# Optimization experiments

Hardware: AMD Instinct MI355X
Metric: run time of the kernel (lower is better)

Reference implementation:

```python
import jax, jax.numpy as jnp
import numpy as np

T, B = 50, 512
S, A, BEL, H, E, M = 256, 32, 1024, 1024, 1024, 256
MIN_STD = 0.1


def setup_inputs() -> dict:
    key = jax.random.key(0)
    ks = jax.random.split(key, 24)
    def rn(k, shape, scale=1.0):
        return jax.random.normal(k, shape, dtype=jnp.float32) * scale
    w = 0.05  # weight init scale
    return {
        "prev_state": rn(ks[0], (B, S)),
        "actions": rn(ks[1], (T, B, A)),
        "prev_belief": rn(ks[2], (B, BEL)),
        "observations": rn(ks[3], (T, B, E)),
        "nonterminals": jnp.ones((T, B, 1), dtype=jnp.float32),
        "map_embeddings": rn(ks[4], (T, B, M)),
        "map_embeddings_post": rn(ks[5], (T, B, M)),
        "noise_prior": rn(ks[6], (T, B, S)),
        "noise_post": rn(ks[7], (T, B, S)),
        "W_sa": rn(ks[8], (BEL, S + A + M), w), "b_sa": jnp.zeros((BEL,), jnp.float32),
        "W_ih": rn(ks[9], (3 * BEL, BEL), w), "b_ih": jnp.zeros((3 * BEL,), jnp.float32),
        "W_hh": rn(ks[10], (3 * BEL, BEL), w), "b_hh": jnp.zeros((3 * BEL,), jnp.float32),
        "W_bp": rn(ks[11], (H, BEL), w), "b_bp": jnp.zeros((H,), jnp.float32),
        "W_sp": rn(ks[12], (2 * S, H), w), "b_sp": jnp.zeros((2 * S,), jnp.float32),
        "W_bq": rn(ks[13], (H, BEL + E + M), w), "b_bq": jnp.zeros((H,), jnp.float32),
        "W_sq": rn(ks[14], (2 * S, H), w), "b_sq": jnp.zeros((2 * S,), jnp.float32),
    }


def reference(prev_state, actions, prev_belief, observations, nonterminals,
              map_embeddings, map_embeddings_post, noise_prior, noise_post,
              W_sa, b_sa, W_ih, b_ih, W_hh, b_hh,
              W_bp, b_bp, W_sp, b_sp, W_bq, b_bq, W_sq, b_sq):
    relu = jax.nn.relu
    def lin(x, W, b):
        return x @ W.T + b

    def gru(x, h):  # torch.nn.GRUCell math
        gi = x @ W_ih.T + b_ih
        gh = h @ W_hh.T + b_hh
        i_r, i_z, i_n = jnp.split(gi, 3, axis=1)
        h_r, h_z, h_n = jnp.split(gh, 3, axis=1)
        r = jax.nn.sigmoid(i_r + h_r)
        z = jax.nn.sigmoid(i_z + h_z)
        n = jnp.tanh(i_n + r * h_n)
        return (1.0 - z) * n + z * h

    def std(raw):
        return jnp.minimum(jax.nn.softplus(raw) + MIN_STD, 5.0)

    def step(carry, xs):
        belief, post_state = carry
        a, obs, nt, me, mp, np_, nq = xs
        s = post_state * nt
        hid = relu(lin(jnp.concatenate([s, a, me], axis=1), W_sa, b_sa))
        belief = gru(hid, belief)
        # prior p(z_t | h_t)
        hp = relu(lin(belief, W_bp, b_bp))
        p_mean, p_raw = jnp.split(lin(hp, W_sp, b_sp), 2, axis=1)
        p_std = std(p_raw)
        p_state = p_mean + p_std * np_
        # posterior q(z_t | h_t, e_t, m_t)
        hq = relu(lin(jnp.concatenate([belief, obs, mp], axis=1), W_bq, b_bq))
        q_mean, q_raw = jnp.split(lin(hq, W_sq, b_sq), 2, axis=1)
        q_std = std(q_raw)
        q_state = q_mean + q_std * nq
        return (belief, q_state), (belief, p_state, p_mean, p_std, q_state, q_mean, q_std)

    _, outs = jax.lax.scan(
        step, (prev_belief, prev_state),
        (actions, observations, nonterminals, map_embeddings,
         map_embeddings_post, noise_prior, noise_post))
    return outs  # 7 arrays, each (T, B, *)
```

## Files before the change

kernel.cpp:

```cpp
#include <hip/hip_runtime.h>
#include <hip/hip_bf16.h>

#define NT 50
#define NB 512
#define SD 256
#define BD 1024
#define HD 1024
#define ED 1024
#define MD 256
#define NBLK 512
#define PGSZ (1024 * 256)
#define K1BIG 0x40000000
#define WPRE_OFF 49152

typedef __attribute__((ext_vector_type(8))) short bf16x8;
typedef __attribute__((ext_vector_type(4))) float f32x4;

__device__ __forceinline__ void gload_lds16(const void* g, void* l) {
  __builtin_amdgcn_global_load_lds(
      (const __attribute__((address_space(1))) void*)g,
      (__attribute__((address_space(3))) void*)l, 16, 0, 0);
}
__device__ __forceinline__ void gload_lds16_sc0(const void* g, void* l) {
  __builtin_amdgcn_global_load_lds(
      (const __attribute__((address_space(1))) void*)g,
      (__attribute__((address_space(3))) void*)l, 16, 0, 1);
}

__device__ __forceinline__ void aload16(const void* a, f32x4* r) {
  asm volatile("global_load_dwordx4 %0, %1, off sc0" : "=&v"(*r) : "v"(a) : "memory");
}
__device__ __forceinline__ void aload4(const void* a, float* r) {
  asm volatile("global_load_dword %0, %1, off sc0" : "=&v"(*r) : "v"(a) : "memory");
}
#define VMWAIT(N)                                        \
  asm volatile("s_waitcnt vmcnt(" #N ")" ::: "memory");  \
  __builtin_amdgcn_sched_barrier(0);

__device__ __forceinline__ void astore16(void* g, f32x4 v) {
  asm volatile("global_store_dwordx4 %0, %1, off sc0" :: "v"(g), "v"(v) : "memory");
}
__device__ __forceinline__ void astore4(void* g, float v) {
  asm volatile("global_store_dword %0, %1, off sc0" :: "v"(g), "v"(v) : "memory");
}
__device__ __forceinline__ void astore2(void* g, unsigned v) {
  asm volatile("global_store_short %0, %1, off sc0" :: "v"(g), "v"(v) : "memory");
}
__device__ __forceinline__ void ntstore16(void* g, f32x4 v) {
  asm volatile("global_store_dwordx4 %0, %1, off nt" :: "v"(g), "v"(v) : "memory");
}
__device__ __forceinline__ void ntstore4(void* g, float v) {
  asm volatile("global_store_dword %0, %1, off nt" :: "v"(g), "v"(v) : "memory");
}

__device__ __forceinline__ float sigmoidf_(float x) { return 1.0f / (1.0f + __expf(-x)); }
__device__ __forceinline__ float softplusf_(float x) {
  return (x > 0.0f) ? (x + log1pf(__expf(-x))) : log1pf(__expf(x));
}
__device__ __forceinline__ unsigned short bfb(float x) {
  __hip_bfloat16 h = __float2bfloat16(x);
  return __builtin_bit_cast(unsigned short, h);
}

__device__ __forceinline__ void wpre_issue(const __hip_bfloat16* W, int ldw,
                                           char* lds, int tid) {
  const int w = tid >> 6, lane = tid & 63;
  const __hip_bfloat16* wrow = W + (size_t)lane * ldw;
  char* wpre = lds + WPRE_OFF;
#pragma unroll
  for (int c = 0; c < 3; ++c) {
    gload_lds16(wrow + (c << 6) + (2 * w) * 8, wpre + c * 8192 + (2 * w) * 1024);
    gload_lds16(wrow + (c << 6) + (2 * w + 1) * 8, wpre + c * 8192 + (2 * w + 1) * 1024);
  }
}

__device__ __forceinline__ void xbar_pf(unsigned* cnt, int inst, int xcd, int nx,
                                        const __hip_bfloat16* nextW, int nextLdw,
                                        char* lds, int tid) {
  asm volatile("s_waitcnt vmcnt(0) lgkmcnt(0)" ::: "memory");
  __syncthreads();
  unsigned* c = cnt + 256 + (size_t)(inst * 8 + xcd) * 16;
  if (tid == 0)
    __hip_atomic_fetch_add(c, 1u, __ATOMIC_RELAXED, __HIP_MEMORY_SCOPE_AGENT);
  if (nextW) wpre_issue(nextW, nextLdw, lds, tid);
  if (tid == 0) {
    while (__hip_atomic_load(c, __ATOMIC_RELAXED, __HIP_MEMORY_SCOPE_AGENT) < (unsigned)nx)
      __builtin_amdgcn_s_sleep(2);
  }
  __syncthreads();
}

__device__ __noinline__ void gemm64(
    int EPI, char* lds, bool pre,
    const __hip_bfloat16* __restrict__ A1, int lda1,
    const __hip_bfloat16* __restrict__ A2, int lda2, int K1,
    const __hip_bfloat16* __restrict__ Wr, int ldw, int nIter,
    const float* __restrict__ bias, const float* __restrict__ Cadd,
    float* __restrict__ Cf, __hip_bfloat16* __restrict__ Cb, int ldc, int m0) {
  const int tid = threadIdx.x;
  const int lane = tid & 63, w = tid >> 6;
  const int wr = w >> 1, wc = w & 1;
  f32x4 acc[2][2] = {};
  const __hip_bfloat16* a1r = A1 + (size_t)(m0 + lane) * lda1;
  const __hip_bfloat16* a2r = A2 ? (A2 + (size_t)(m0 + lane) * lda2) : a1r;
  const __hip_bfloat16* wrow = Wr + (size_t)lane * ldw;
  char* wpre = lds + WPRE_OFF;

  auto aissue = [&](int it) {
    const int k0 = it << 6;
    char* la = lds + (size_t)(it % 3) * 16384;
    const __hip_bfloat16* as = (k0 < K1) ? (a1r + k0) : (a2r + (k0 - K1));
    gload_lds16_sc0(as + (2 * w) * 8, la + (2 * w) * 1024);
    gload_lds16_sc0(as + (2 * w + 1) * 8, la + (2 * w + 1) * 1024);
  };
  auto stageAW = [&](int it) {
    const int k0 = it << 6;
    char* la = lds + (size_t)(it % 3) * 16384;
    char* lb = la + 8192;
    const __hip_bfloat16* as = (k0 < K1) ? (a1r + k0) : (a2r + (k0 - K1));
    gload_lds16_sc0(as + (2 * w) * 8, la + (2 * w) * 1024);
    gload_lds16_sc0(as + (2 * w + 1) * 8, la + (2 * w + 1) * 1024);
    gload_lds16(wrow + k0 + (2 * w) * 8, lb + (2 * w) * 1024);
    gload_lds16(wrow + k0 + (2 * w + 1) * 8, lb + (2 * w + 1) * 1024);
  };

  __syncthreads();
  if (!pre) wpre_issue(Wr, ldw, lds, tid);
  aissue(0);
  aissue(1);
  aissue(2);
  VMWAIT(4)
  __builtin_amdgcn_s_barrier();
  __builtin_amdgcn_sched_barrier(0);

  const int kq = lane >> 4, r15 = lane & 15;
  for (int i = 0; i < nIter; ++i) {
    const char* la = lds + (size_t)(i % 3) * 16384;
    const char* lb = (i < 3) ? (wpre + (size_t)i * 8192) : (la + 8192);
#pragma unroll
    for (int s = 0; s < 2; ++s) {
      bf16x8 af[2], bfr[2];
#pragma unroll
      for (int m = 0; m < 2; ++m)
        af[m] = *(const bf16x8*)(la + (size_t)((s * 4 + kq) * 64 + wr * 32 + m * 16 + r15) * 16);
#pragma unroll
      for (int n = 0; n < 2; ++n)
        bfr[n] = *(const bf16x8*)(lb + (size_t)((s * 4 + kq) * 64 + wc * 32 + n * 16 + r15) * 16);
#pragma unroll
      for (int m = 0; m < 2; ++m)
#pragma unroll
        for (int n = 0; n < 2; ++n)
          acc[m][n] = __builtin_amdgcn_mfma_f32_16x16x32_bf16(af[m], bfr[n], acc[m][n], 0, 0, 0);
    }
    if (i + 1 < nIter) {
      if (i == 0) {
        VMWAIT(2)
      } else if (i + 2 < nIter) {
        VMWAIT(4)
      } else {
        VMWAIT(0)
      }
      __builtin_amdgcn_s_barrier();
      __builtin_amdgcn_sched_barrier(0);
      if (i + 3 < nIter) stageAW(i + 3);
    }
  }

  const int rg = lane >> 4;
  float ad[2][2][4];
  if (EPI == 3) {
#pragma unroll
    for (int m = 0; m < 2; ++m)
#pragma unroll
      for (int n = 0; n < 2; ++n) {
        const int col = wc * 32 + n * 16 + r15;
#pragma unroll
        for (int i2 = 0; i2 < 4; ++i2) {
          const int row = m0 + wr * 32 + m * 16 + rg * 4 + i2;
          aload4(Cadd + (size_t)row * ldc + col, &ad[m][n][i2]);
        }
      }
    VMWAIT(0)
  }
#pragma unroll
  for (int m = 0; m < 2; ++m) {
#pragma unroll
    for (int n = 0; n < 2; ++n) {
      const int col = wc * 32 + n * 16 + r15;
      const float bv = bias ? bias[col] : 0.0f;
#pragma unroll
      for (int i2 = 0; i2 < 4; ++i2) {
        const int row = m0 + wr * 32 + m * 16 + rg * 4 + i2;
        float v = acc[m][n][i2] + bv;
        if (EPI == 3) v += ad[m][n][i2];
        if (EPI == 0) {
          astore4(Cf + (size_t)row * ldc + col, v);
        } else {
          v = v > 0.0f ? v : 0.0f;
          astore2(Cb + (size_t)row * ldc + col, (unsigned)bfb(v));
        }
      }
    }
  }
}

__device__ __noinline__ void gemm_head64(
    char* lds, bool pre, const __hip_bfloat16* __restrict__ A,
    const __hip_bfloat16* __restrict__ Wr, const float* __restrict__ bias,
    const float* __restrict__ noise, float* __restrict__ st_o, float* __restrict__ mn_o,
    float* __restrict__ sd_o, const float* __restrict__ ntn,
    __hip_bfloat16* __restrict__ sprev, int isq, int n0, int m0) {
  const int tid = threadIdx.x;
  const int lane = tid & 63, w = tid >> 6;
  const int wr = w >> 1, wc = w & 1;
  f32x4 acc[2][2] = {};
  const __hip_bfloat16* ar = A + (size_t)(m0 + lane) * BD;
  const __hip_bfloat16* wrow = Wr + (size_t)lane * BD;
  char* wpre = lds + WPRE_OFF;

  auto aissue = [&](int it) {
    const int k0 = it << 6;
    char* la = lds + (size_t)(it % 3) * 16384;
    gload_lds16_sc0(ar + k0 + (2 * w) * 8, la + (2 * w) * 1024);
    gload_lds16_sc0(ar + k0 + (2 * w + 1) * 8, la + (2 * w + 1) * 1024);
  };
  auto stageAW = [&](int it) {
    const int k0 = it << 6;
    char* la = lds + (size_t)(it % 3) * 16384;
    char* lb = la + 8192;
    gload_lds16_sc0(ar + k0 + (2 * w) * 8, la + (2 * w) * 1024);
    gload_lds16_sc0(ar + k0 + (2 * w + 1) * 8, la + (2 * w + 1) * 1024);
    gload_lds16(wrow + k0 + (2 * w) * 8, lb + (2 * w) * 1024);
    gload_lds16(wrow + k0 + (2 * w + 1) * 8, lb + (2 * w + 1) * 1024);
  };

  __syncthreads();
  if (!pre) wpre_issue(Wr, BD, lds, tid);
  aissue(0);
  aissue(1);
  aissue(2);
  VMWAIT(4)
  __builtin_amdgcn_s_barrier();
  __builtin_amdgcn_sched_barrier(0);

  const int kq = lane >> 4, r15 = lane & 15;
  for (int i = 0; i < 16; ++i) {
    const char* la = lds + (size_t)(i % 3) * 16384;
    const char* lb = (i < 3) ? (wpre + (size_t)i * 8192) : (la + 8192);
#pragma unroll
    for (int s = 0; s < 2; ++s) {
      bf16x8 af[2], bfr[2];
#pragma unroll
      for (int m = 0; m < 2; ++m)
        af[m] = *(const bf16x8*)(la + (size_t)((s * 4 + kq) * 64 + wr * 32 + m * 16 + r15) * 16);
#pragma unroll
      for (int n = 0; n < 2; ++n)
        bfr[n] = *(const bf16x8*)(lb + (size_t)((s * 4 + kq) * 64 + wc * 32 + n * 16 + r15) * 16);
#pragma unroll
      for (int m = 0; m < 2; ++m)
#pragma unroll
        for (int n = 0; n < 2; ++n)
          acc[m][n] = __builtin_amdgcn_mfma_f32_16x16x32_bf16(af[m], bfr[n], acc[m][n], 0, 0, 0);
    }
    if (i + 1 < 16) {
      if (i == 0) {
        VMWAIT(2)
      } else if (i + 2 < 16) {
        VMWAIT(4)
      } else {
        VMWAIT(0)
      }
      __builtin_amdgcn_s_barrier();
      __builtin_amdgcn_sched_barrier(0);
      if (i + 3 < 16) stageAW(i + 3);
    }
  }

  const int rg = lane >> 4;
  const bool even = (r15 & 1) == 0;
#pragma unroll
  for (int m = 0; m < 2; ++m) {
#pragma unroll
    for (int n = 0; n < 2; ++n) {
      const int col = n0 + wc * 32 + n * 16 + r15;
      const int j = col >> 1;
      const float bv = bias[col];
#pragma unroll
      for (int i2 = 0; i2 < 4; ++i2) {
        const int row = m0 + wr * 32 + m * 16 + rg * 4 + i2;
        float v = acc[m][n][i2] + bv;
        float partner = __shfl_xor(v, 1);
        float mean = even ? v : partner;
        float raw = even ? partner : v;
        float sd = fminf(softplusf_(raw) + 0.1f, 5.0f);
        const size_t o = (size_t)row * SD + j;
        if (even) {
          float st = mean + sd * noise[o];
          ntstore4(mn_o + o, mean);
          ntstore4(st_o + o, st);
          if (isq) astore2(sprev + o, (unsigned)bfb(st * ntn[row]));
        } else {
          ntstore4(sd_o + o, sd);
        }
      }
    }
  }
}

struct Args {
  const float *prev_state, *actions, *prev_belief, *observations, *nonterminals,
      *me, *mp, *noise_p, *noise_q,
      *W_sa, *b_sa, *W_ih, *b_ih, *W_hh, *b_hh,
      *W_bp, *b_bp, *W_sp, *b_sp, *W_bq, *b_bq, *W_sq, *b_sq;
  float* out;
  unsigned* cnt;
  __hip_bfloat16 *Wsa, *Wih, *Whh, *Wbp, *Wbq, *Wsp, *Wsq;
  __hip_bfloat16 *actme, *obsmp, *sprev, *bel, *hid, *hpb, *hqb;
  float *gi, *gh, *hq_obs;
  float *bsp_ro, *bsq_ro;
};

__global__ __launch_bounds__(256) void prep(Args P) {
  const int gtid = blockIdx.x * 256 + threadIdx.x;
  for (int i = gtid; i < BD * 576; i += PGSZ) {
    int r = i / 576, k = i - r * 576;
    P.Wsa[i] = __float2bfloat16(k < 544 ? P.W_sa[(size_t)r * 544 + k] : 0.0f);
  }
  for (int i = gtid; i < 3 * BD * BD; i += PGSZ) P.Wih[i] = __float2bfloat16(P.W_ih[i]);
  for (int i = gtid; i < 3 * BD * BD; i += PGSZ) P.Whh[i] = __float2bfloat16(P.W_hh[i]);
  for (int i = gtid; i < HD * BD; i += PGSZ) P.Wbp[i] = __float2bfloat16(P.W_bp[i]);
  for (int i = gtid; i < HD * 2304; i += PGSZ) P.Wbq[i] = __float2bfloat16(P.W_bq[i]);
  for (int i = gtid; i < 512 * HD; i += PGSZ) {
    int r = i >> 10, k = i & 1023;
    int dr = (r < 256) ? (2 * r) : (2 * (r - 256) + 1);
    P.Wsp[(size_t)dr * 1024 + k] = __float2bfloat16(P.W_sp[i]);
    P.Wsq[(size_t)dr * 1024 + k] = __float2bfloat16(P.W_sq[i]);
  }
  for (int i = gtid; i < 512; i += PGSZ) {
    int dr = (i < 256) ? (2 * i) : (2 * (i - 256) + 1);
    P.bsp_ro[dr] = P.b_sp[i];
    P.bsq_ro[dr] = P.b_sq[i];
  }
  for (int i = gtid; i < NT * NB * 320; i += PGSZ) {
    int tb = i / 320, j = i - tb * 320;
    float v = (j < 32) ? P.actions[(size_t)tb * 32 + j]
                       : (j < 288 ? P.me[(size_t)tb * 256 + (j - 32)] : 0.0f);
    P.actme[i] = __float2bfloat16(v);
  }
  for (int i = gtid; i < NB * 1280; i += PGSZ) {
    int bb = i / 1280, j = i - bb * 1280;
    float v = (j < ED) ? P.observations[(size_t)bb * ED + j] : P.mp[(size_t)bb * MD + (j - ED)];
    P.obsmp[i] = __float2bfloat16(v);
  }
  for (int i = gtid; i < NB * SD; i += PGSZ) {
    int r = i >> 8;
    P.sprev[i] = __float2bfloat16(P.prev_state[i] * P.nonterminals[r]);
  }
  for (int i = gtid; i < NB * BD; i += PGSZ) P.bel[i] = __float2bfloat16(P.prev_belief[i]);
}

__global__ __launch_bounds__(256, 2) void mega(Args P) {
  __shared__ alignas(16) char lds[73728];
  __shared__ int sh[4];
  const int tid = threadIdx.x;

  if (tid == 0) {
    unsigned x;
    asm volatile("s_getreg_b32 %0, hwreg(HW_REG_XCC_ID)" : "=s"(x));
    x &= 7u;
    unsigned s = __hip_atomic_fetch_add(P.cnt + x * 16, 1u, __ATOMIC_RELAXED,
                                        __HIP_MEMORY_SCOPE_AGENT);
    sh[0] = (int)x;
    sh[1] = (int)s;
  }
  __syncthreads();
  const int xcd = sh[0], slot = sh[1];

  if (tid == 0) {
    __hip_atomic_fetch_add(P.cnt + 128, 1u, __ATOMIC_RELAXED, __HIP_MEMORY_SCOPE_AGENT);
    while (__hip_atomic_load(P.cnt + 128, __ATOMIC_RELAXED, __HIP_MEMORY_SCOPE_AGENT) <
           (unsigned)NBLK)
      __builtin_amdgcn_s_sleep(4);
    sh[2] = (int)__hip_atomic_load(P.cnt + xcd * 16, __ATOMIC_RELAXED,
                                   __HIP_MEMORY_SCOPE_AGENT);
  }
  __syncthreads();
  const int nx = sh[2];
  const int m0 = xcd * 64;
  const size_t o_ps = (size_t)NT * NB * BD;
  const size_t blk = (size_t)NT * NB * SD;

  const __hip_bfloat16* wA = nullptr; int lA = 0;
  if (slot < 16) { wA = P.Wsa + (size_t)slot * 64 * 576; lA = 576; }
  else if (slot < 64) { wA = P.Whh + (size_t)(slot - 16) * 64 * BD; lA = BD; }
  const __hip_bfloat16* wB = nullptr; int lB = 0;
  if (slot < 48) { wB = P.Wih + (size_t)slot * 64 * BD; lB = BD; }
  else if (slot < 64) { wB = P.Wbq + (size_t)(slot - 48) * 64 * 2304 + 1024; lB = 2304; }
  const __hip_bfloat16* wD = nullptr; int lD = 0;
  if (slot < 16) { wD = P.Wbp + (size_t)slot * 64 * BD; lD = BD; }
  else if (slot < 32) { wD = P.Wbq + (size_t)(slot - 16) * 64 * 2304; lD = 2304; }
  const __hip_bfloat16* wE = nullptr; int lE = 0;
  if (slot < 8) { wE = P.Wsp + (size_t)slot * 64 * BD; lE = BD; }
  else if (slot < 16) { wE = P.Wsq + (size_t)(slot - 8) * 64 * BD; lE = BD; }

  if (wA) wpre_issue(wA, lA, lds, tid);

  for (int t = 0; t < NT; ++t) {
    const int inst = t * 5;
    for (int tt = slot; tt < 64; tt += nx) {
      const bool pre = (tt == slot);
      if (tt < 16) {
        gemm64(1, lds, pre, P.sprev, SD, P.actme + (size_t)t * NB * 320, 320, 256,
               P.Wsa + (size_t)tt * 64 * 576, 576, 9,
               P.b_sa + tt * 64, nullptr, nullptr, P.hid + tt * 64, BD, m0);
      } else {
        const int n = tt - 16;
        gemm64(0, lds, pre, P.bel, BD, nullptr, 0, K1BIG,
               P.Whh + (size_t)n * 64 * BD, BD, 16,
               P.b_hh + n * 64, nullptr, P.gh + n * 64, nullptr, 3 * BD, m0);
      }
    }
    xbar_pf(P.cnt, inst + 0, xcd, nx, wB, lB, lds, tid);
    for (int tt = slot; tt < 64; tt += nx) {
      const bool pre = (tt == slot);
      if (tt < 48) {
        gemm64(0, lds, pre, P.hid, BD, nullptr, 0, K1BIG,
               P.Wih + (size_t)tt * 64 * BD, BD, 16,
               P.b_ih + tt * 64, nullptr, P.gi + tt * 64, nullptr, 3 * BD, m0);
      } else {
        const int n = tt - 48;
        gemm64(0, lds, pre, P.obsmp, 1280, nullptr, 0, K1BIG,
               P.Wbq + (size_t)n * 64 * 2304 + 1024, 2304, 20,
               nullptr, nullptr, P.hq_obs + n * 64, nullptr, 1024, m0);
      }
    }
    xbar_pf(P.cnt, inst + 1, xcd, nx, wD, lD, lds, tid);
    for (int u = slot * 256 + tid; u < 8192; u += nx * 256) {
      const int r = m0 + (u >> 7), j0 = (u & 127) << 3;
      const float* gib = P.gi + (size_t)r * 3072 + j0;
      const float* ghb = P.gh + (size_t)r * 3072 + j0;
      f32x4 ir0, ir1, iz0, iz1, in0, in1, hr0, hr1, hz0, hz1, hn0, hn1, hbv;
      aload16(gib, &ir0);
      aload16(gib + 4, &ir1);
      aload16(gib + 1024, &iz0);
      aload16(gib + 1028, &iz1);
      aload16(gib + 2048, &in0);
      aload16(gib + 2052, &in1);
      aload16(ghb, &hr0);
      aload16(ghb + 4, &hr1);
      aload16(ghb + 1024, &hz0);
      aload16(ghb + 1028, &hz1);
      aload16(ghb + 2048, &hn0);
      aload16(ghb + 2052, &hn1);
      aload16(P.bel + (size_t)r * BD + j0, &hbv);
      VMWAIT(0)
      bf16x8 hb = __builtin_bit_cast(bf16x8, hbv);
      float o[8];
      unsigned short nb[8];
#pragma unroll
      for (int k = 0; k < 8; ++k) {
        float gr = (k < 4 ? ir0[k] : ir1[k - 4]) + (k < 4 ? hr0[k] : hr1[k - 4]);
        float gz = (k < 4 ? iz0[k] : iz1[k - 4]) + (k < 4 ? hz0[k] : hz1[k - 4]);
        float hn = (k < 4 ? hn0[k] : hn1[k - 4]);
        float in_ = (k < 4 ? in0[k] : in1[k - 4]);
        float r_ = sigmoidf_(gr);
        float z_ = sigmoidf_(gz);
        float n_ = tanhf(in_ + r_ * hn);
        __hip_bfloat16 hv16 = __builtin_bit_cast(__hip_bfloat16, (unsigned short)hb[k]);
        float hv = __bfloat162float(hv16);
        float bel = (1.0f - z_) * n_ + z_ * hv;
        o[k] = bel;
        nb[k] = bfb(bel);
      }
      float* ob = P.out + (size_t)t * NB * BD + (size_t)r * BD + j0;
      ntstore16(ob, f32x4{o[0], o[1], o[2], o[3]});
      ntstore16(ob + 4, f32x4{o[4], o[5], o[6], o[7]});
      astore16(P.bel + (size_t)r * BD + j0, __builtin_bit_cast(f32x4, *(bf16x8*)nb));
    }
    if (t + 1 < NT) {
      for (int v = slot * 256 + tid; v < 5120; v += nx * 256) {
        const int r = m0 + v / 80, c0 = (v % 80) << 4;
        const float* src = (c0 < ED)
            ? (P.observations + (size_t)(t + 1) * NB * ED + (size_t)r * ED + c0)
            : (P.mp + (size_t)(t + 1) * NB * MD + (size_t)r * MD + (c0 - ED));
        unsigned short nb[16];
#pragma unroll
        for (int q = 0; q < 4; ++q) {
          f32x4 vv = *(const f32x4*)(src + q * 4);
#pragma unroll
          for (int kk = 0; kk < 4; ++kk) nb[q * 4 + kk] = bfb(vv[kk]);
        }
        astore16(P.obsmp + (size_t)r * 1280 + c0, __builtin_bit_cast(f32x4, *(bf16x8*)nb));
        astore16(P.obsmp + (size_t)r * 1280 + c0 + 8,
                 __builtin_bit_cast(f32x4, *(bf16x8*)(nb + 8)));
      }
    }
    xbar_pf(P.cnt, inst + 2, xcd, nx, nullptr, 0, lds, tid);
    for (int tt = slot; tt < 32; tt += nx) {
      const bool pre = (tt == slot);
      if (tt < 16) {
        gemm64(1, lds, pre, P.bel, BD, nullptr, 0, K1BIG,
               P.Wbp + (size_t)tt * 64 * BD, BD, 16,
               P.b_bp + tt * 64, nullptr, nullptr, P.hpb + tt * 64, HD, m0);
      } else {
        const int n = tt - 16;
        gemm64(3, lds, pre, P.bel, BD, nullptr, 0, K1BIG,
               P.Wbq + (size_t)n * 64 * 2304, 2304, 16,
               P.b_bq + n * 64, P.hq_obs + n * 64, nullptr, P.hqb + n * 64, HD, m0);
      }
    }
    xbar_pf(P.cnt, inst + 3, xcd, nx, wE, lE, lds, tid);
    {
      const float* ntn = P.nonterminals + (size_t)((t + 1 < NT) ? t + 1 : t) * NB;
      const size_t to = (size_t)t * NB * SD;
      for (int tt = slot; tt < 16; tt += nx) {
        const bool pre = (tt == slot);
        if (tt < 8)
          gemm_head64(lds, pre, P.hpb, P.Wsp + (size_t)tt * 64 * BD, P.bsp_ro,
                      P.noise_p + to, P.out + o_ps + to, P.out + o_ps + blk + to,
                      P.out + o_ps + 2 * blk + to, ntn, P.sprev, 0, tt * 64, m0);
        else
          gemm_head64(lds, pre, P.hqb, P.Wsq + (size_t)(tt - 8) * 64 * BD, P.bsq_ro,
                      P.noise_q + to, P.out + o_ps + 3 * blk + to,
                      P.out + o_ps + 4 * blk + to, P.out + o_ps + 5 * blk + to,
                      ntn, P.sprev, 1, (tt - 8) * 64, m0);
      }
    }
    xbar_pf(P.cnt, inst + 4, xcd, nx, wA, lA, lds, tid);
  }
}


extern "C" void kernel_launch(void* const* d_in, const int* in_sizes, int n_in,
                              void* d_out, int out_size, void* d_ws, size_t ws_size,
                              hipStream_t stream) {
  Args P;
  P.prev_state = (const float*)d_in[0];
  P.actions = (const float*)d_in[1];
  P.prev_belief = (const float*)d_in[2];
  P.observations = (const float*)d_in[3];
  P.nonterminals = (const float*)d_in[4];
  P.me = (const float*)d_in[5];
  P.mp = (const float*)d_in[6];
  P.noise_p = (const float*)d_in[7];
  P.noise_q = (const float*)d_in[8];
  P.W_sa = (const float*)d_in[9];  P.b_sa = (const float*)d_in[10];
  P.W_ih = (const float*)d_in[11]; P.b_ih = (const float*)d_in[12];
  P.W_hh = (const float*)d_in[13]; P.b_hh = (const float*)d_in[14];
  P.W_bp = (const float*)d_in[15]; P.b_bp = (const float*)d_in[16];
  P.W_sp = (const float*)d_in[17]; P.b_sp = (const float*)d_in[18];
  P.W_bq = (const float*)d_in[19]; P.b_bq = (const float*)d_in[20];
  P.W_sq = (const float*)d_in[21]; P.b_sq = (const float*)d_in[22];
  P.out = (float*)d_out;

  char* p = (char*)d_ws;
  auto carve = [&](size_t bytes) -> char* {
    char* r = p;
    p += (bytes + 255) & ~(size_t)255;
    return r;
  };
  const size_t cnt_bytes = (size_t)65536 * 4;
  P.cnt = (unsigned*)carve(cnt_bytes);
  P.Wsa = (__hip_bfloat16*)carve((size_t)BD * 576 * 2);
  P.Wih = (__hip_bfloat16*)carve((size_t)3 * BD * BD * 2);
  P.Whh = (__hip_bfloat16*)carve((size_t)3 * BD * BD * 2);
  P.Wbp = (__hip_bfloat16*)carve((size_t)HD * BD * 2);
  P.Wbq = (__hip_bfloat16*)carve((size_t)HD * 2304 * 2);
  P.Wsp = (__hip_bfloat16*)carve((size_t)512 * HD * 2);
  P.Wsq = (__hip_bfloat16*)carve((size_t)512 * HD * 2);
  P.bsp_ro = (float*)carve(512 * 4);
  P.bsq_ro = (float*)carve(512 * 4);
  P.actme = (__hip_bfloat16*)carve((size_t)NT * NB * 320 * 2);
  P.obsmp = (__hip_bfloat16*)carve((size_t)NB * 1280 * 2);
  P.sprev = (__hip_bfloat16*)carve((size_t)NB * SD * 2);
  P.bel = (__hip_bfloat16*)carve((size_t)NB * BD * 2);
  P.hid = (__hip_bfloat16*)carve((size_t)NB * BD * 2);
  P.hpb = (__hip_bfloat16*)carve((size_t)NB * HD * 2);
  P.hqb = (__hip_bfloat16*)carve((size_t)NB * HD * 2);
  P.gi = (float*)carve((size_t)NB * 3 * BD * 4);
  P.gh = (float*)carve((size_t)NB * 3 * BD * 4);
  P.hq_obs = (float*)carve((size_t)NB * HD * 4);

  hipMemsetAsync(P.cnt, 0, cnt_bytes, stream);
  prep<<<1024, 256, 0, stream>>>(P);
  mega<<<NBLK, 256, 0, stream>>>(P);
}
```

Measured before the change: 5.319 ms.

## Fuse GRU gate GEMMs with cell update and hoist observation projection out of recurrence

The observation/map part of the posterior projection does not depend on the recurrence, so it is now computed for all timesteps in a separate batched pre-kernel (preg) into a bf16 buffer. GRU input and hidden weights are reordered so each tile holds the r/z/n rows for the same 16 units. A new gemm_gru routine computes both gate GEMMs and applies the cell update in its epilogue, removing the fp32 gi/gh round trip and one grid barrier per step. Belief is double-buffered so the in-place update does not race. In exchange the kernel uses more workspace (all-timestep obs and hq buffers), stores the precomputed projection in bf16, and GRU tiles are 48 wide with some wasted lanes.

After: 5.379 ms. About the same (+1.1%).

```diff
diff --git a/kernel.cpp b/kernel.cpp
--- a/kernel.cpp
+++ b/kernel.cpp
@@ -33,6 +33,9 @@
 __device__ __forceinline__ void aload4(const void* a, float* r) {
   asm volatile("global_load_dword %0, %1, off sc0" : "=&v"(*r) : "v"(a) : "memory");
 }
+__device__ __forceinline__ void aload2(const void* a, unsigned* r) {
+  asm volatile("global_load_ushort %0, %1, off sc0" : "=&v"(*r) : "v"(a) : "memory");
+}
 #define VMWAIT(N)                                        \
   asm volatile("s_waitcnt vmcnt(" #N ")" ::: "memory");  \
   __builtin_amdgcn_sched_barrier(0);
@@ -46,9 +49,6 @@
 __device__ __forceinline__ void astore2(void* g, unsigned v) {
   asm volatile("global_store_short %0, %1, off sc0" :: "v"(g), "v"(v) : "memory");
 }
-__device__ __forceinline__ void ntstore16(void* g, f32x4 v) {
-  asm volatile("global_store_dwordx4 %0, %1, off nt" :: "v"(g), "v"(v) : "memory");
-}
 __device__ __forceinline__ void ntstore4(void* g, float v) {
   asm volatile("global_store_dword %0, %1, off nt" :: "v"(g), "v"(v) : "memory");
 }
@@ -60,6 +60,10 @@
 __device__ __forceinline__ unsigned short bfb(float x) {
   __hip_bfloat16 h = __float2bfloat16(x);
   return __builtin_bit_cast(unsigned short, h);
+}
+__device__ __forceinline__ float b2f(unsigned short u) {
+  __hip_bfloat16 h = __builtin_bit_cast(__hip_bfloat16, u);
+  return __bfloat162float(h);
 }
 
 __device__ __forceinline__ void wpre_issue(const __hip_bfloat16* W, int ldw,
@@ -95,8 +99,8 @@
     const __hip_bfloat16* __restrict__ A1, int lda1,
     const __hip_bfloat16* __restrict__ A2, int lda2, int K1,
     const __hip_bfloat16* __restrict__ Wr, int ldw, int nIter,
-    const float* __restrict__ bias, const float* __restrict__ Cadd,
-    float* __restrict__ Cf, __hip_bfloat16* __restrict__ Cb, int ldc, int m0) {
+    const float* __restrict__ bias, const void* __restrict__ Cadd,
+    __hip_bfloat16* __restrict__ Cb, int ldc, int m0) {
   const int tid = threadIdx.x;
   const int lane = tid & 63, w = tid >> 6;
   const int wr = w >> 1, wc = w & 1;
@@ -167,8 +171,8 @@
   }
 
   const int rg = lane >> 4;
-  float ad[2][2][4];
-  if (EPI == 3) {
+  unsigned adu[2][2][4];
+  if (EPI == 5) {
 #pragma unroll
     for (int m = 0; m < 2; ++m)
 #pragma unroll
@@ -177,7 +181,7 @@
 #pragma unroll
         for (int i2 = 0; i2 < 4; ++i2) {
           const int row = m0 + wr * 32 + m * 16 + rg * 4 + i2;
-          aload4(Cadd + (size_t)row * ldc + col, &ad[m][n][i2]);
+          aload2((const unsigned short*)Cadd + (size_t)row * ldc + col, &adu[m][n][i2]);
         }
       }
     VMWAIT(0)
@@ -192,15 +196,89 @@
       for (int i2 = 0; i2 < 4; ++i2) {
         const int row = m0 + wr * 32 + m * 16 + rg * 4 + i2;
         float v = acc[m][n][i2] + bv;
-        if (EPI == 3) v += ad[m][n][i2];
-        if (EPI == 0) {
-          astore4(Cf + (size_t)row * ldc + col, v);
-        } else {
-          v = v > 0.0f ? v : 0.0f;
-          astore2(Cb + (size_t)row * ldc + col, (unsigned)bfb(v));
-        }
-      }
-    }
+        if (EPI == 5) v += b2f((unsigned short)adu[m][n][i2]);
+        if (EPI != 4) v = v > 0.0f ? v : 0.0f;
+        astore2(Cb + (size_t)row * ldc + col, (unsigned)bfb(v));
+      }
+    }
+  }
+}
+
+__device__ __noinline__ void gemm_gru(
+    char* lds, const __hip_bfloat16* __restrict__ Wih3,
+    const __hip_bfloat16* __restrict__ Whh3,
+    const float* __restrict__ b_ih, const float* __restrict__ b_hh,
+    const __hip_bfloat16* __restrict__ hid, const __hip_bfloat16* __restrict__ belR,
+    __hip_bfloat16* __restrict__ belW, float* __restrict__ outT, int n, int m0) {
+  const int tid = threadIdx.x;
+  const int lane = tid & 63, w = tid >> 6;
+  f32x4 agi[3] = {}, agh[3] = {};
+  const __hip_bfloat16* hrow = hid + (size_t)(m0 + lane) * BD;
+  const __hip_bfloat16* brow = belR + (size_t)(m0 + lane) * BD;
+  const int wln = (lane < 48) ? lane : 47;
+  const __hip_bfloat16* wirow = Wih3 + (size_t)(n * 48 + wln) * BD;
+  const __hip_bfloat16* whrow = Whh3 + (size_t)(n * 48 + wln) * BD;
+
+  auto stage = [&](int it) {
+    const int k0 = it << 5;
+    char* buf = lds + (size_t)(it % 3) * 16384;
+    gload_lds16_sc0(hrow + k0 + w * 8, buf + w * 1024);
+    gload_lds16_sc0(brow + k0 + w * 8, buf + 4096 + w * 1024);
+    gload_lds16(wirow + k0 + w * 8, buf + 8192 + w * 1024);
+    gload_lds16(whrow + k0 + w * 8, buf + 12288 + w * 1024);
+  };
+
+  __syncthreads();
+  stage(0);
+  stage(1);
+  VMWAIT(4)
+  __builtin_amdgcn_s_barrier();
+  __builtin_amdgcn_sched_barrier(0);
+
+  const int kq = lane >> 4, r15 = lane & 15;
+  for (int i = 0; i < 32; ++i) {
+    if (i + 2 < 32) stage(i + 2);
+    const char* buf = lds + (size_t)(i % 3) * 16384;
+    bf16x8 ah = *(const bf16x8*)(buf + (size_t)(kq * 64 + w * 16 + r15) * 16);
+    bf16x8 ab = *(const bf16x8*)(buf + 4096 + (size_t)(kq * 64 + w * 16 + r15) * 16);
+#pragma unroll
+    for (int g = 0; g < 3; ++g) {
+      bf16x8 wi = *(const bf16x8*)(buf + 8192 + (size_t)(kq * 64 + g * 16 + r15) * 16);
+      bf16x8 wh = *(const bf16x8*)(buf + 12288 + (size_t)(kq * 64 + g * 16 + r15) * 16);
+      agi[g] = __builtin_amdgcn_mfma_f32_16x16x32_bf16(ah, wi, agi[g], 0, 0, 0);
+      agh[g] = __builtin_amdgcn_mfma_f32_16x16x32_bf16(ab, wh, agh[g], 0, 0, 0);
+    }
+    if (i + 1 < 32) {
+      if (i + 2 < 32) {
+        VMWAIT(4)
+      } else {
+        VMWAIT(0)
+      }
+      __builtin_amdgcn_s_barrier();
+      __builtin_amdgcn_sched_barrier(0);
+    }
+  }
+
+  const int rg = lane >> 4;
+  const int unit = n * 16 + r15;
+  const int rowb = m0 + w * 16 + rg * 4;
+  const float bir = b_ih[unit], biz = b_ih[1024 + unit], bin = b_ih[2048 + unit];
+  const float bhr = b_hh[unit], bhz = b_hh[1024 + unit], bhn = b_hh[2048 + unit];
+  unsigned hp4[4];
+#pragma unroll
+  for (int i = 0; i < 4; ++i)
+    aload2(belR + (size_t)(rowb + i) * BD + unit, &hp4[i]);
+  VMWAIT(0)
+#pragma unroll
+  for (int i = 0; i < 4; ++i) {
+    const int row = rowb + i;
+    float r_ = sigmoidf_((agi[0][i] + bir) + (agh[0][i] + bhr));
+    float z_ = sigmoidf_((agi[1][i] + biz) + (agh[1][i] + bhz));
+    float n_ = tanhf((agi[2][i] + bin) + r_ * (agh[2][i] + bhn));
+    float hv = b2f((unsigned short)hp4[i]);
+    float bel = (1.0f - z_) * n_ + z_ * hv;
+    ntstore4(outT + (size_t)row * BD + unit, bel);
+    astore2(belW + (size_t)row * BD + unit, (unsigned)bfb(bel));
   }
 }
 
@@ -314,9 +392,8 @@
       *W_bp, *b_bp, *W_sp, *b_sp, *W_bq, *b_bq, *W_sq, *b_sq;
   float* out;
   unsigned* cnt;
-  __hip_bfloat16 *Wsa, *Wih, *Whh, *Wbp, *Wbq, *Wsp, *Wsq;
-  __hip_bfloat16 *actme, *obsmp, *sprev, *bel, *hid, *hpb, *hqb;
-  float *gi, *gh, *hq_obs;
+  __hip_bfloat16 *Wsa, *Wih3, *Whh3, *Wbp, *Wbq, *Wsp, *Wsq;
+  __hip_bfloat16 *actme, *obsall, *hqall, *sprev, *belA, *belB, *hid, *hpb, *hqb;
   float *bsp_ro, *bsq_ro;
 };
 
@@ -326,8 +403,13 @@
     int r = i / 576, k = i - r * 576;
     P.Wsa[i] = __float2bfloat16(k < 544 ? P.W_sa[(size_t)r * 544 + k] : 0.0f);
   }
-  for (int i = gtid; i < 3 * BD * BD; i += PGSZ) P.Wih[i] = __float2bfloat16(P.W_ih[i]);
-  for (int i = gtid; i < 3 * BD * BD; i += PGSZ) P.Whh[i] = __float2bfloat16(P.W_hh[i]);
+  for (int i = gtid; i < 3 * BD * BD; i += PGSZ) {
+    int rp = i >> 10, k = i & 1023;
+    int n = rp / 48, rem = rp - n * 48, g = rem >> 4, u = rem & 15;
+    size_t src = (size_t)(g * 1024 + n * 16 + u) * 1024 + k;
+    P.Wih3[i] = __float2bfloat16(P.W_ih[src]);
+    P.Whh3[i] = __float2bfloat16(P.W_hh[src]);
+  }
   for (int i = gtid; i < HD * BD; i += PGSZ) P.Wbp[i] = __float2bfloat16(P.W_bp[i]);
   for (int i = gtid; i < HD * 2304; i += PGSZ) P.Wbq[i] = __float2bfloat16(P.W_bq[i]);
   for (int i = gtid; i < 512 * HD; i += PGSZ) {
@@ -347,21 +429,30 @@
                        : (j < 288 ? P.me[(size_t)tb * 256 + (j - 32)] : 0.0f);
     P.actme[i] = __float2bfloat16(v);
   }
-  for (int i = gtid; i < NB * 1280; i += PGSZ) {
-    int bb = i / 1280, j = i - bb * 1280;
-    float v = (j < ED) ? P.observations[(size_t)bb * ED + j] : P.mp[(size_t)bb * MD + (j - ED)];
-    P.obsmp[i] = __float2bfloat16(v);
+  for (size_t i = gtid; i < (size_t)NT * NB * 1280; i += PGSZ) {
+    size_t tb = i / 1280;
+    int j = (int)(i - tb * 1280);
+    float v = (j < ED) ? P.observations[tb * ED + j] : P.mp[tb * MD + (j - ED)];
+    P.obsall[i] = __float2bfloat16(v);
   }
   for (int i = gtid; i < NB * SD; i += PGSZ) {
     int r = i >> 8;
     P.sprev[i] = __float2bfloat16(P.prev_state[i] * P.nonterminals[r]);
   }
-  for (int i = gtid; i < NB * BD; i += PGSZ) P.bel[i] = __float2bfloat16(P.prev_belief[i]);
+  for (int i = gtid; i < NB * BD; i += PGSZ) P.belA[i] = __float2bfloat16(P.prev_belief[i]);
+}
+
+__global__ __launch_bounds__(256, 2) void preg(Args P) {
+  __shared__ alignas(16) char lds[73728];
+  const int mt = blockIdx.x % 400, nt = blockIdx.x / 400;
+  gemm64(4, lds, false, P.obsall, 1280, nullptr, 0, K1BIG,
+         P.Wbq + (size_t)nt * 64 * 2304 + 1024, 2304, 20,
+         nullptr, nullptr, P.hqall + nt * 64, 1024, mt * 64);
 }
 
 __global__ __launch_bounds__(256, 2) void mega(Args P) {
   __shared__ alignas(16) char lds[73728];
-  __shared__ int sh[4];
+  __shared__ int sh[3];
   const int tid = threadIdx.x;
 
   if (tid == 0) {
@@ -390,12 +481,8 @@
   const size_t o_ps = (size_t)NT * NB * BD;
   const size_t blk = (size_t)NT * NB * SD;
 
-  const __hip_bfloat16* wA = nullptr; int lA = 0;
-  if (slot < 16) { wA = P.Wsa + (size_t)slot * 64 * 576; lA = 576; }
-  else if (slot < 64) { wA = P.Whh + (size_t)(slot - 16) * 64 * BD; lA = BD; }
-  const __hip_bfloat16* wB = nullptr; int lB = 0;
-  if (slot < 48) { wB = P.Wih + (size_t)slot * 64 * BD; lB = BD; }
-  else if (slot < 64) { wB = P.Wbq + (size_t)(slot - 48) * 64 * 2304 + 1024; lB = 2304; }
+  const __hip_bfloat16* wA = (slot < 16) ? P.Wsa + (size_t)slot * 64 * 576 : nullptr;
+  const int lA = 576;
   const __hip_bfloat16* wD = nullptr; int lD = 0;
   if (slot < 16) { wD = P.Wbp + (size_t)slot * 64 * BD; lD = BD; }
   else if (slot < 32) { wD = P.Wbq + (size_t)(slot - 16) * 64 * 2304; lD = 2304; }
@@ -406,110 +493,35 @@
   if (wA) wpre_issue(wA, lA, lds, tid);
 
   for (int t = 0; t < NT; ++t) {
-    const int inst = t * 5;
+    const int inst = t * 4;
+    const __hip_bfloat16* belR = (t & 1) ? P.belB : P.belA;
+    __hip_bfloat16* belW = (t & 1) ? P.belA : P.belB;
+    for (int tt = slot; tt < 16; tt += nx) {
+      gemm64(1, lds, tt == slot, P.sprev, SD, P.actme + (size_t)t * NB * 320, 320, 256,
+             P.Wsa + (size_t)tt * 64 * 576, 576, 9,
+             P.b_sa + tt * 64, nullptr, P.hid + tt * 64, BD, m0);
+    }
+    xbar_pf(P.cnt, inst + 0, xcd, nx, nullptr, 0, lds, tid);
     for (int tt = slot; tt < 64; tt += nx) {
-      const bool pre = (tt == slot);
-      if (tt < 16) {
-        gemm64(1, lds, pre, P.sprev, SD, P.actme + (size_t)t * NB * 320, 320, 256,
-               P.Wsa + (size_t)tt * 64 * 576, 576, 9,
-               P.b_sa + tt * 64, nullptr, nullptr, P.hid + tt * 64, BD, m0);
-      } else {
-        const int n = tt - 16;
-        gemm64(0, lds, pre, P.bel, BD, nullptr, 0, K1BIG,
-               P.Whh + (size_t)n * 64 * BD, BD, 16,
-               P.b_hh + n * 64, nullptr, P.gh + n * 64, nullptr, 3 * BD, m0);
-      }
-    }
-    xbar_pf(P.cnt, inst + 0, xcd, nx, wB, lB, lds, tid);
-    for (int tt = slot; tt < 64; tt += nx) {
-      const bool pre = (tt == slot);
-      if (tt < 48) {
-        gemm64(0, lds, pre, P.hid, BD, nullptr, 0, K1BIG,
-               P.Wih + (size_t)tt * 64 * BD, BD, 16,
-               P.b_ih + tt * 64, nullptr, P.gi + tt * 64, nullptr, 3 * BD, m0);
-      } else {
-        const int n = tt - 48;
-        gemm64(0, lds, pre, P.obsmp, 1280, nullptr, 0, K1BIG,
-               P.Wbq + (size_t)n * 64 * 2304 + 1024, 2304, 20,
-               nullptr, nullptr, P.hq_obs + n * 64, nullptr, 1024, m0);
-      }
+      gemm_gru(lds, P.Wih3, P.Whh3, P.b_ih, P.b_hh, P.hid, belR, belW,
+               P.out + (size_t)t * NB * BD, tt, m0);
     }
     xbar_pf(P.cnt, inst + 1, xcd, nx, wD, lD, lds, tid);
-    for (int u = slot * 256 + tid; u < 8192; u += nx * 256) {
-      const int r = m0 + (u >> 7), j0 = (u & 127) << 3;
-      const float* gib = P.gi + (size_t)r * 3072 + j0;
-      const float* ghb = P.gh + (size_t)r * 3072 + j0;
-      f32x4 ir0, ir1, iz0, iz1, in0, in1, hr0, hr1, hz0, hz1, hn0, hn1, hbv;
-      aload16(gib, &ir0);
-      aload16(gib + 4, &ir1);
-      aload16(gib + 1024, &iz0);
-      aload16(gib + 1028, &iz1);
-      aload16(gib + 2048, &in0);
-      aload16(gib + 2052, &in1);
-      aload16(ghb, &hr0);
-      aload16(ghb + 4, &hr1);
-      aload16(ghb + 1024, &hz0);
-      aload16(ghb + 1028, &hz1);
-      aload16(ghb + 2048, &hn0);
-      aload16(ghb + 2052, &hn1);
-      aload16(P.bel + (size_t)r * BD + j0, &hbv);
-      VMWAIT(0)
-      bf16x8 hb = __builtin_bit_cast(bf16x8, hbv);
-      float o[8];
-      unsigned short nb[8];
-#pragma unroll
-      for (int k = 0; k < 8; ++k) {
-        float gr = (k < 4 ? ir0[k] : ir1[k - 4]) + (k < 4 ? hr0[k] : hr1[k - 4]);
-        float gz = (k < 4 ? iz0[k] : iz1[k - 4]) + (k < 4 ? hz0[k] : hz1[k - 4]);
-        float hn = (k < 4 ? hn0[k] : hn1[k - 4]);
-        float in_ = (k < 4 ? in0[k] : in1[k - 4]);
-        float r_ = sigmoidf_(gr);
-        float z_ = sigmoidf_(gz);
-        float n_ = tanhf(in_ + r_ * hn);
-        __hip_bfloat16 hv16 = __builtin_bit_cast(__hip_bfloat16, (unsigned short)hb[k]);
-        float hv = __bfloat162float(hv16);
-        float bel = (1.0f - z_) * n_ + z_ * hv;
-        o[k] = bel;
-        nb[k] = bfb(bel);
-      }
-      float* ob = P.out + (size_t)t * NB * BD + (size_t)r * BD + j0;
-      ntstore16(ob, f32x4{o[0], o[1], o[2], o[3]});
-      ntstore16(ob + 4, f32x4{o[4], o[5], o[6], o[7]});
-      astore16(P.bel + (size_t)r * BD + j0, __builtin_bit_cast(f32x4, *(bf16x8*)nb));
-    }
-    if (t + 1 < NT) {
-      for (int v = slot * 256 + tid; v < 5120; v += nx * 256) {
-        const int r = m0 + v / 80, c0 = (v % 80) << 4;
-        const float* src = (c0 < ED)
-            ? (P.observations + (size_t)(t + 1) * NB * ED + (size_t)r * ED + c0)
-            : (P.mp + (size_t)(t + 1) * NB * MD + (size_t)r * MD + (c0 - ED));
-        unsigned short nb[16];
-#pragma unroll
-        for (int q = 0; q < 4; ++q) {
-          f32x4 vv = *(const f32x4*)(src + q * 4);
-#pragma unroll
-          for (int kk = 0; kk < 4; ++kk) nb[q * 4 + kk] = bfb(vv[kk]);
-        }
-        astore16(P.obsmp + (size_t)r * 1280 + c0, __builtin_bit_cast(f32x4, *(bf16x8*)nb));
-        astore16(P.obsmp + (size_t)r * 1280 + c0 + 8,
-                 __builtin_bit_cast(f32x4, *(bf16x8*)(nb + 8)));
-      }
-    }
-    xbar_pf(P.cnt, inst + 2, xcd, nx, nullptr, 0, lds, tid);
     for (int tt = slot; tt < 32; tt += nx) {
       const bool pre = (tt == slot);
       if (tt < 16) {
-        gemm64(1, lds, pre, P.bel, BD, nullptr, 0, K1BIG,
+        gemm64(1, lds, pre, belW, BD, nullptr, 0, K1BIG,
                P.Wbp + (size_t)tt * 64 * BD, BD, 16,
-               P.b_bp + tt * 64, nullptr, nullptr, P.hpb + tt * 64, HD, m0);
+               P.b_bp + tt * 64, nullptr, P.hpb + tt * 64, HD, m0);
       } else {
         const int n = tt - 16;
-        gemm64(3, lds, pre, P.bel, BD, nullptr, 0, K1BIG,
+        gemm64(5, lds, pre, belW, BD, nullptr, 0, K1BIG,
                P.Wbq + (size_t)n * 64 * 2304, 2304, 16,
-               P.b_bq + n * 64, P.hq_obs + n * 64, nullptr, P.hqb + n * 64, HD, m0);
-      }
-    }
-    xbar_pf(P.cnt, inst + 3, xcd, nx, wE, lE, lds, tid);
+               P.b_bq + n * 64, P.hqall + (size_t)t * NB * HD + n * 64,
+               P.hqb + n * 64, HD, m0);
+      }
+    }
+    xbar_pf(P.cnt, inst + 2, xcd, nx, wE, lE, lds, tid);
     {
       const float* ntn = P.nonterminals + (size_t)((t + 1 < NT) ? t + 1 : t) * NB;
       const size_t to = (size_t)t * NB * SD;
@@ -526,7 +538,7 @@
                       ntn, P.sprev, 1, (tt - 8) * 64, m0);
       }
     }
-    xbar_pf(P.cnt, inst + 4, xcd, nx, wA, lA, lds, tid);
+    xbar_pf(P.cnt, inst + 3, xcd, nx, wA, lA, lds, tid);
   }
 }
 
@@ -562,8 +574,8 @@
   const size_t cnt_bytes = (size_t)65536 * 4;
   P.cnt = (unsigned*)carve(cnt_bytes);
   P.Wsa = (__hip_bfloat16*)carve((size_t)BD * 576 * 2);
-  P.Wih = (__hip_bfloat16*)carve((size_t)3 * BD * BD * 2);
-  P.Whh = (__hip_bfloat16*)carve((size_t)3 * BD * BD * 2);
+  P.Wih3 = (__hip_bfloat16*)carve((size_t)3 * BD * BD * 2);
+  P.Whh3 = (__hip_bfloat16*)carve((size_t)3 * BD * BD * 2);
   P.Wbp = (__hip_bfloat16*)carve((size_t)HD * BD * 2);
   P.Wbq = (__hip_bfloat16*)carve((size_t)HD * 2304 * 2);
   P.Wsp = (__hip_bfloat16*)carve((size_t)512 * HD * 2);
@@ -571,17 +583,17 @@
   P.bsp_ro = (float*)carve(512 * 4);
   P.bsq_ro = (float*)carve(512 * 4);
   P.actme = (__hip_bfloat16*)carve((size_t)NT * NB * 320 * 2);
-  P.obsmp = (__hip_bfloat16*)carve((size_t)NB * 1280 * 2);
+  P.obsall = (__hip_bfloat16*)carve((size_t)NT * NB * 1280 * 2);
+  P.hqall = (__hip_bfloat16*)carve((size_t)NT * NB * HD * 2);
   P.sprev = (__hip_bfloat16*)carve((size_t)NB * SD * 2);
-  P.bel = (__hip_bfloat16*)carve((size_t)NB * BD * 2);
+  P.belA = (__hip_bfloat16*)carve((size_t)NB * BD * 2);
+  P.belB = (__hip_bfloat16*)carve((size_t)NB * BD * 2);
   P.hid = (__hip_bfloat16*)carve((size_t)NB * BD * 2);
   P.hpb = (__hip_bfloat16*)carve((size_t)NB * HD * 2);
   P.hqb = (__hip_bfloat16*)carve((size_t)NB * HD * 2);
-  P.gi = (float*)carve((size_t)NB * 3 * BD * 4);
-  P.gh = (float*)carve((size_t)NB * 3 * BD * 4);
-  P.hq_obs = (float*)carve((size_t)NB * HD * 4);
 
   hipMemsetAsync(P.cnt, 0, cnt_bytes, stream);
   prep<<<1024, 256, 0, stream>>>(P);
+  preg<<<6400, 256, 0, stream>>>(P);
   mega<<<NBLK, 256, 0, stream>>>(P);
 }
```
